# Performance work log

Measured on AMD Instinct MI355X. Metric: run time of the kernel, lower is better.

The kernel has to match this reference:

```python
import jax, jax.numpy as jnp
import numpy as np

EMBED = 1024
NHEAD = 16
HEAD_DIM = EMBED // NHEAD
DFF = 4096
TOP_K = 64
LN_EPS = 1e-5


def _layernorm(x, g, b):
    mu = jnp.mean(x, axis=-1, keepdims=True)
    var = jnp.var(x, axis=-1, keepdims=True)
    return (x - mu) * jax.lax.rsqrt(var + LN_EPS) * g + b


def setup_inputs() -> dict:
    key = jax.random.key(0)
    ks = jax.random.split(key, 12)
    s = 0.02
    return {
        "x": jax.random.normal(ks[0], (2, 2048, EMBED), dtype=jnp.float32),
        "Wq": jax.random.normal(ks[1], (EMBED, EMBED), dtype=jnp.float32) * s,
        "bq": jnp.zeros((EMBED,), jnp.float32),
        "Wk": jax.random.normal(ks[2], (EMBED, EMBED), dtype=jnp.float32) * s,
        "bk": jnp.zeros((EMBED,), jnp.float32),
        "Wv": jax.random.normal(ks[3], (EMBED, EMBED), dtype=jnp.float32) * s,
        "bv": jnp.zeros((EMBED,), jnp.float32),
        "Wo": jax.random.normal(ks[4], (EMBED, EMBED), dtype=jnp.float32) * s,
        "bo": jnp.zeros((EMBED,), jnp.float32),
        "g1": jnp.ones((EMBED,), jnp.float32),
        "be1": jnp.zeros((EMBED,), jnp.float32),
        "g2": jnp.ones((EMBED,), jnp.float32),
        "be2": jnp.zeros((EMBED,), jnp.float32),
        "W1": jax.random.normal(ks[5], (EMBED, DFF), dtype=jnp.float32) * s,
        "b1": jnp.zeros((DFF,), jnp.float32),
        "W2": jax.random.normal(ks[6], (DFF, EMBED), dtype=jnp.float32) * s,
        "b2": jnp.zeros((EMBED,), jnp.float32),
    }


def reference(x, Wq, bq, Wk, bk, Wv, bv, Wo, bo, g1, be1, g2, be2, W1, b1, W2, b2):
    B, N, E = x.shape
    res = x
    h = _layernorm(x, g1, be1)
    # [B, H, N, D]
    q = (h @ Wq + bq).reshape(B, N, NHEAD, HEAD_DIM).transpose(0, 2, 1, 3)
    k = (h @ Wk + bk).reshape(B, N, NHEAD, HEAD_DIM).transpose(0, 2, 1, 3)
    v = (h @ Wv + bv).reshape(B, N, NHEAD, HEAD_DIM).transpose(0, 2, 1, 3)
    scores = jnp.einsum("bhqd,bhkd->bhqk", q, k) / jnp.sqrt(jnp.float32(HEAD_DIM))
    if TOP_K < N:
        topv, _ = jax.lax.top_k(scores, TOP_K)  # [B,H,N,TOP_K]
        thresh = topv[..., -1:, ]
        scores = jnp.where(scores < thresh, -jnp.inf, scores)
    attn = jax.nn.softmax(scores, axis=-1)
    out = jnp.einsum("bhqk,bhkd->bhqd", attn, v)
    out = out.transpose(0, 2, 1, 3).reshape(B, N, E)
    out = out @ Wo + bo
    x1 = res + out  # dropout is identity at eval
    h2 = _layernorm(x1, g2, be2)
    ff = jax.nn.gelu(h2 @ W1 + b1, approximate=False) @ W2 + b2
    return x1 + ff
```

## Files before the change

### kernel.cpp

```cpp
#include <hip/hip_runtime.h>

typedef short short8v __attribute__((ext_vector_type(8)));
typedef float floatx4 __attribute__((ext_vector_type(4)));
typedef unsigned short us4 __attribute__((ext_vector_type(4)));

#define EMB 1024
#define QKVW 3072
#define SEQ 2048
#define NH 16
#define HD 64
#define TOPK 64
#define QBLK 16
#define CAP 128
#define SROW 2056
#define ATTN_SMEM (QBLK * SROW * 2 + QBLK * CAP * 4)

#define GLDS16(gp, lp)                                                        \
  __builtin_amdgcn_global_load_lds(                                           \
      (const __attribute__((address_space(1))) void*)(gp),                    \
      (__attribute__((address_space(3))) void*)(lp), 16, 0, 0)

static __device__ __forceinline__ unsigned short f2b(float f) {
  union { float f; unsigned u; } in; in.f = f;
  unsigned u = in.u;
  return (unsigned short)((u + 0x7FFFu + ((u >> 16) & 1u)) >> 16);
}
static __device__ __forceinline__ float b2f(unsigned short b) {
  union { unsigned u; float f; } o; o.u = ((unsigned)b) << 16;
  return o.f;
}
static __device__ __forceinline__ unsigned mmap(unsigned s) {
  return (s & 0x8000u) ? (~s & 0xFFFFu) : (s | 0x8000u);
}
static __device__ __forceinline__ unsigned short munmap(unsigned u) {
  return (u & 0x8000u) ? (unsigned short)(u ^ 0x8000u) : (unsigned short)(~u & 0xFFFFu);
}

__global__ __launch_bounds__(256) void ln_kernel(const float* __restrict__ X,
    const float* __restrict__ gam, const float* __restrict__ bet,
    unsigned short* __restrict__ H) {
  const int row = blockIdx.x;
  const int tid = threadIdx.x;
  const float4 v = *(const float4*)&X[(size_t)row * EMB + tid * 4];
  float s1 = v.x + v.y + v.z + v.w;
  float s2 = v.x * v.x + v.y * v.y + v.z * v.z + v.w * v.w;
#pragma unroll
  for (int off = 32; off; off >>= 1) { s1 += __shfl_xor(s1, off); s2 += __shfl_xor(s2, off); }
  __shared__ float red[2][4];
  const int w = tid >> 6, l = tid & 63;
  if (l == 0) { red[0][w] = s1; red[1][w] = s2; }
  __syncthreads();
  s1 = red[0][0] + red[0][1] + red[0][2] + red[0][3];
  s2 = red[1][0] + red[1][1] + red[1][2] + red[1][3];
  const float mu = s1 * (1.f / EMB);
  const float var = s2 * (1.f / EMB) - mu * mu;
  const float rs = rsqrtf(var + 1e-5f);
  const float4 gv = *(const float4*)&gam[tid * 4];
  const float4 bv = *(const float4*)&bet[tid * 4];
  us4 o;
  o.x = f2b((v.x - mu) * rs * gv.x + bv.x);
  o.y = f2b((v.y - mu) * rs * gv.y + bv.y);
  o.z = f2b((v.z - mu) * rs * gv.z + bv.z);
  o.w = f2b((v.w - mu) * rs * gv.w + bv.w);
  *(us4*)&H[(size_t)row * EMB + tid * 4] = o;
}

__global__ __launch_bounds__(256) void wcvt_kernel(const float* __restrict__ W,
    unsigned short* __restrict__ WT, int K, int N) {
  __shared__ unsigned short t[64][72];
  const int n0 = blockIdx.x * 64, k0 = blockIdx.y * 64;
  const int tid = threadIdx.x;
#pragma unroll
  for (int i = 0; i < 4; ++i) {
    const int f = i * 256 + tid;
    const int k = f >> 4, n4 = (f & 15) * 4;
    const float4 v = *(const float4*)&W[(size_t)(k0 + k) * N + n0 + n4];
    t[n4 + 0][k] = f2b(v.x);
    t[n4 + 1][k] = f2b(v.y);
    t[n4 + 2][k] = f2b(v.z);
    t[n4 + 3][k] = f2b(v.w);
  }
  __syncthreads();
#pragma unroll
  for (int i = 0; i < 2; ++i) {
    const int f = i * 256 + tid;
    const int n = f >> 3, c8 = (f & 7) * 8;
    short8v o;
#pragma unroll
    for (int j = 0; j < 8; ++j) o[j] = (short)t[n][c8 + j];
    *(short8v*)&WT[(size_t)(n0 + n) * K + k0 + c8] = o;
  }
}

static __device__ __forceinline__ void xcd_tile(int& bm, int& bn) {
  const int gx = gridDim.x;
  const int nwg = gx * gridDim.y;
  const int flat = blockIdx.y * gx + blockIdx.x;
  const int q8 = nwg >> 3;
  const int wg = (flat & 7) * q8 + (flat >> 3);
  bm = (wg / gx) * 128;
  bn = (wg % gx) * 128;
}

template <int EPI>
__global__ __launch_bounds__(256) void gemm_bt4_kernel(
    const unsigned short* __restrict__ A, const unsigned short* __restrict__ BT,
    const float* __restrict__ bias, const float* __restrict__ res,
    void* __restrict__ Cout, int M, int N, int K) {
  __shared__ __align__(16) unsigned short lA[128 * 32];
  __shared__ __align__(16) unsigned short lB[128 * 32];
  const int tid = threadIdx.x;
  const int l = tid & 63, w = tid >> 6;
  const int wm = (w >> 1) * 64, wn = (w & 1) * 64;
  int bm, bn; xcd_tile(bm, bn);
  const int g = l >> 4, r16 = l & 15;
  const int lr = l >> 2, lc = (l & 3) * 8;
  floatx4 acc[4][4] = {};
  for (int kt = 0; kt < K; kt += 32) {
#pragma unroll
    for (int j = 0; j < 2; ++j) {
      GLDS16(&A[(size_t)(bm + w * 32 + j * 16 + lr) * K + kt + lc],
             &lA[(w * 32 + j * 16) * 32]);
      GLDS16(&BT[(size_t)(bn + w * 32 + j * 16 + lr) * K + kt + lc],
             &lB[(w * 32 + j * 16) * 32]);
    }
    __syncthreads();
    short8v a[4], b[4];
#pragma unroll
    for (int m = 0; m < 4; ++m) a[m] = *(const short8v*)&lA[(wm + m * 16 + r16) * 32 + g * 8];
#pragma unroll
    for (int n = 0; n < 4; ++n) b[n] = *(const short8v*)&lB[(wn + n * 16 + r16) * 32 + g * 8];
#pragma unroll
    for (int m = 0; m < 4; ++m)
#pragma unroll
      for (int n = 0; n < 4; ++n)
        acc[m][n] = __builtin_amdgcn_mfma_f32_16x16x32_bf16(a[m], b[n], acc[m][n], 0, 0, 0);
    __syncthreads();
  }
#pragma unroll
  for (int m = 0; m < 4; ++m) {
#pragma unroll
    for (int n = 0; n < 4; ++n) {
#pragma unroll
      for (int r = 0; r < 4; ++r) {
        const int gm = bm + wm + m * 16 + g * 4 + r;
        const int gn = bn + wn + n * 16 + r16;
        float v = acc[m][n][r] + bias[gn];
        if constexpr (EPI == 0) {
          ((unsigned short*)Cout)[(size_t)gm * N + gn] = f2b(v);
        } else if constexpr (EPI == 1) {
          const float ge = 0.5f * v * (1.f + erff(v * 0.70710678118f));
          ((unsigned short*)Cout)[(size_t)gm * N + gn] = f2b(ge);
        } else {
          ((float*)Cout)[(size_t)gm * N + gn] = v + res[(size_t)gm * N + gn];
        }
      }
    }
  }
}

template <int EPI>
__global__ __launch_bounds__(512) void gemm_bt8_kernel(
    const unsigned short* __restrict__ A, const unsigned short* __restrict__ BT,
    const float* __restrict__ bias, const float* __restrict__ res,
    void* __restrict__ Cout, int M, int N, int K) {
  __shared__ __align__(16) unsigned short lA[128 * 32];
  __shared__ __align__(16) unsigned short lB[128 * 32];
  const int tid = threadIdx.x;
  const int l = tid & 63, w = tid >> 6;
  const int wm = (w & 1) * 64, wn = (w >> 1) * 32;
  int bm, bn; xcd_tile(bm, bn);
  const int g = l >> 4, r16 = l & 15;
  const int lr = l >> 2, lc = (l & 3) * 8;
  floatx4 acc[4][2] = {};
  for (int kt = 0; kt < K; kt += 32) {
    GLDS16(&A[(size_t)(bm + w * 16 + lr) * K + kt + lc], &lA[(w * 16) * 32]);
    GLDS16(&BT[(size_t)(bn + w * 16 + lr) * K + kt + lc], &lB[(w * 16) * 32]);
    __syncthreads();
    short8v a[4], b[2];
#pragma unroll
    for (int m = 0; m < 4; ++m) a[m] = *(const short8v*)&lA[(wm + m * 16 + r16) * 32 + g * 8];
#pragma unroll
    for (int n = 0; n < 2; ++n) b[n] = *(const short8v*)&lB[(wn + n * 16 + r16) * 32 + g * 8];
#pragma unroll
    for (int m = 0; m < 4; ++m)
#pragma unroll
      for (int n = 0; n < 2; ++n)
        acc[m][n] = __builtin_amdgcn_mfma_f32_16x16x32_bf16(a[m], b[n], acc[m][n], 0, 0, 0);
    __syncthreads();
  }
#pragma unroll
  for (int m = 0; m < 4; ++m) {
#pragma unroll
    for (int n = 0; n < 2; ++n) {
#pragma unroll
      for (int r = 0; r < 4; ++r) {
        const int gm = bm + wm + m * 16 + g * 4 + r;
        const int gn = bn + wn + n * 16 + r16;
        float v = acc[m][n][r] + bias[gn];
        if constexpr (EPI == 0) {
          ((unsigned short*)Cout)[(size_t)gm * N + gn] = f2b(v);
        } else if constexpr (EPI == 1) {
          const float ge = 0.5f * v * (1.f + erff(v * 0.70710678118f));
          ((unsigned short*)Cout)[(size_t)gm * N + gn] = f2b(ge);
        } else {
          ((float*)Cout)[(size_t)gm * N + gn] = v + res[(size_t)gm * N + gn];
        }
      }
    }
  }
}

__global__ __launch_bounds__(1024, 8) void attn_kernel(
    const unsigned short* __restrict__ qkv, unsigned short* __restrict__ O) {
  extern __shared__ unsigned short smem[];
  unsigned short (*scores)[SROW] = (unsigned short(*)[SROW])smem;
  unsigned* hist = (unsigned*)(smem + QBLK * SROW);

  const int tid = threadIdx.x;
  const int l = tid & 63, w = tid >> 6;
  const int g = l >> 4, r16 = l & 15;
  const int qb = blockIdx.x;
  const int h = blockIdx.y;
  const int bz = blockIdx.z;
  const size_t rowbase = (size_t)bz * SEQ;
  const int hcol = h * HD;

  ((uint2*)hist)[tid] = uint2{0u, 0u};

  {
    const size_t qrow = (rowbase + qb * QBLK + r16) * QKVW + hcol;
    const short8v a0 = *(const short8v*)&qkv[qrow + g * 8];
    const short8v a1 = *(const short8v*)&qkv[qrow + 32 + g * 8];
    const int kbase = w * 128;
#pragma unroll 2
    for (int kti = 0; kti < 8; ++kti) {
      const int key0 = kbase + kti * 16;
      const size_t krow = (rowbase + key0 + r16) * QKVW + 1024 + hcol;
      const short8v b0 = *(const short8v*)&qkv[krow + g * 8];
      const short8v b1 = *(const short8v*)&qkv[krow + 32 + g * 8];
      floatx4 acc = {0.f, 0.f, 0.f, 0.f};
      acc = __builtin_amdgcn_mfma_f32_16x16x32_bf16(a0, b0, acc, 0, 0, 0);
      acc = __builtin_amdgcn_mfma_f32_16x16x32_bf16(a1, b1, acc, 0, 0, 0);
#pragma unroll
      for (int r = 0; r < 4; ++r)
        scores[g * 4 + r][key0 + r16] = (unsigned short)mmap(f2b(acc[r] * 0.125f));
    }
  }
  __syncthreads();

  const unsigned long long ltmask = (1ull << l) - 1ull;
  const int half = l >> 5, dl = l & 31;
  const int q = w;
  unsigned* srow32 = (unsigned*)&scores[q][0];
  unsigned* comp = &hist[q * CAP];

  unsigned ux[16];
  unsigned um = 0;
#pragma unroll
  for (int i = 0; i < 16; ++i) {
    const unsigned x = srow32[l + 64 * i];
    ux[i] = x;
    const unsigned u0 = x & 0xFFFFu, u1 = x >> 16;
    const unsigned mx = (u0 > u1) ? u0 : u1;
    um = (mx > um) ? mx : um;
  }
#pragma unroll
  for (int off = 32; off; off >>= 1) {
    const unsigned o2 = (unsigned)__shfl_xor((int)um, off);
    um = (o2 > um) ? o2 : um;
  }
  const float mf = b2f(munmap(um));

#pragma unroll
  for (int i = 0; i < 16; ++i) {
    const unsigned d0 = um - (ux[i] & 0xFFFFu);
    const unsigned d1 = um - (ux[i] >> 16);
    if (d0 < 256u) atomicAdd(&comp[d0 >> 1], 1u << ((d0 & 1u) * 16));
    if (d1 < 256u) atomicAdd(&comp[d1 >> 1], 1u << ((d1 & 1u) * 16));
  }
  asm volatile("s_waitcnt lgkmcnt(0)" ::: "memory");
  unsigned ut;
  {
    const unsigned w0 = comp[2 * l], w1 = comp[2 * l + 1];
    const unsigned c0 = w0 & 0xFFFFu, c1 = w0 >> 16, c2 = w1 & 0xFFFFu, c3 = w1 >> 16;
    const unsigned s4 = c0 + c1 + c2 + c3;
    unsigned incl = s4;
#pragma unroll
    for (int off = 1; off < 64; off <<= 1) {
      const unsigned t2 = (unsigned)__shfl_up((int)incl, off);
      if (l >= off) incl += t2;
    }
    const unsigned pre = incl - s4;
    unsigned dc = 0xFFFFFFFFu;
    if      (pre + c0 >= TOPK)           dc = 4 * l;
    else if (pre + c0 + c1 >= TOPK)      dc = 4 * l + 1;
    else if (pre + c0 + c1 + c2 >= TOPK) dc = 4 * l + 2;
    else if (incl >= TOPK)               dc = 4 * l + 3;
#pragma unroll
    for (int off = 32; off; off >>= 1) {
      const unsigned o2 = (unsigned)__shfl_xor((int)dc, off);
      dc = (o2 < dc) ? o2 : dc;
    }
    if (dc != 0xFFFFFFFFu) {
      ut = um - dc;
    } else {
      unsigned t = 0;
#pragma unroll 1
      for (int bit = 15; bit >= 0; --bit) {
        const unsigned cand = t | (1u << bit);
        int c = 0;
#pragma unroll
        for (int i = 0; i < 16; ++i) {
          c += __popcll(__ballot((ux[i] & 0xFFFFu) >= cand));
          c += __popcll(__ballot((ux[i] >> 16) >= cand));
        }
        if (c >= TOPK) t = cand;
      }
      ut = t;
    }
  }

  float lsum = 0.f;
  unsigned base = 0;
#pragma unroll
  for (int i = 0; i < 16; ++i) {
    const unsigned u0 = ux[i] & 0xFFFFu, u1 = ux[i] >> 16;
    const bool k0 = (u0 >= ut), k1 = (u1 >= ut);
    const float e0 = k0 ? __expf(b2f(munmap(u0)) - mf) : 0.f;
    const float e1 = k1 ? __expf(b2f(munmap(u1)) - mf) : 0.f;
    lsum += e0 + e1;
    const unsigned key0 = 2 * (l + 64 * i);
    const unsigned long long m0 = __ballot(k0);
    if (k0) {
      const unsigned pos = base + (unsigned)__popcll(m0 & ltmask);
      if (pos < CAP) comp[pos] = (key0 << 16) | (unsigned)f2b(e0);
    }
    base += (unsigned)__popcll(m0);
    const unsigned long long m1 = __ballot(k1);
    if (k1) {
      const unsigned pos = base + (unsigned)__popcll(m1 & ltmask);
      if (pos < CAP) comp[pos] = ((key0 + 1) << 16) | (unsigned)f2b(e1);
    }
    base += (unsigned)__popcll(m1);
  }
#pragma unroll
  for (int off = 32; off; off >>= 1) lsum += __shfl_xor(lsum, off);
  const float rinv = 1.f / lsum;
  const unsigned cntc = (base < CAP) ? base : CAP;

  const unsigned short* vbase = &qkv[rowbase * QKVW + 2048 + hcol + dl * 2];
  float ox = 0.f, oy = 0.f;
#pragma unroll 4
  for (unsigned k = 0; k < 64; k += 2) {
    const unsigned c = comp[k + half];
    const float p = b2f((unsigned short)(c & 0xFFFFu));
    const unsigned idx = c >> 16;
    const unsigned vv = *(const unsigned*)&vbase[(size_t)idx * QKVW];
    ox += p * b2f((unsigned short)(vv & 0xFFFFu));
    oy += p * b2f((unsigned short)(vv >> 16));
  }
#pragma unroll 1
  for (unsigned k = 64; k < cntc; k += 2) {
    const unsigned kk = k + half;
    const unsigned c = (kk < cntc) ? comp[kk] : 0u;
    const float p = b2f((unsigned short)(c & 0xFFFFu));
    const unsigned idx = c >> 16;
    const unsigned vv = *(const unsigned*)&vbase[(size_t)idx * QKVW];
    ox += p * b2f((unsigned short)(vv & 0xFFFFu));
    oy += p * b2f((unsigned short)(vv >> 16));
  }
  ox += __shfl_xor(ox, 32);
  oy += __shfl_xor(oy, 32);
  if (l < 32) {
    const unsigned ow = (unsigned)f2b(ox * rinv) | ((unsigned)f2b(oy * rinv) << 16);
    *(unsigned*)&O[(rowbase + qb * QBLK + q) * EMB + hcol + dl * 2] = ow;
  }
}

extern "C" void kernel_launch(void* const* d_in, const int* in_sizes, int n_in,
                              void* d_out, int out_size, void* d_ws, size_t ws_size,
                              hipStream_t stream) {
  (void)in_sizes; (void)n_in; (void)out_size; (void)ws_size;
  const float* x  = (const float*)d_in[0];
  const float* Wq = (const float*)d_in[1];
  const float* bq = (const float*)d_in[2];
  const float* Wk = (const float*)d_in[3];
  const float* bk = (const float*)d_in[4];
  const float* Wv = (const float*)d_in[5];
  const float* bv = (const float*)d_in[6];
  const float* Wo = (const float*)d_in[7];
  const float* bo = (const float*)d_in[8];
  const float* g1 = (const float*)d_in[9];
  const float* be1 = (const float*)d_in[10];
  const float* g2 = (const float*)d_in[11];
  const float* be2 = (const float*)d_in[12];
  const float* W1 = (const float*)d_in[13];
  const float* b1 = (const float*)d_in[14];
  const float* W2 = (const float*)d_in[15];
  const float* b2 = (const float*)d_in[16];
  float* out = (float*)d_out;

  char* ws = (char*)d_ws;
  float* x1 = (float*)ws;
  unsigned short* hbuf  = (unsigned short*)(ws + ((size_t)16 << 20));
  unsigned short* qkvb  = (unsigned short*)(ws + ((size_t)24 << 20));
  unsigned short* Ob    = (unsigned short*)(ws + ((size_t)48 << 20));
  unsigned short* ff1   = (unsigned short*)(ws + ((size_t)24 << 20));
  float* bqkv           = (float*)(ws + ((size_t)48 << 20));
  unsigned short* WqkvT = (unsigned short*)(ws + ((size_t)56 << 20));
  unsigned short* WoT   = (unsigned short*)(ws + ((size_t)62 << 20));
  unsigned short* W1T   = (unsigned short*)(ws + ((size_t)64 << 20));
  unsigned short* W2T   = (unsigned short*)(ws + ((size_t)72 << 20));

  hipMemcpyAsync(bqkv,        bq, 1024 * 4, hipMemcpyDeviceToDevice, stream);
  hipMemcpyAsync(bqkv + 1024, bk, 1024 * 4, hipMemcpyDeviceToDevice, stream);
  hipMemcpyAsync(bqkv + 2048, bv, 1024 * 4, hipMemcpyDeviceToDevice, stream);

  wcvt_kernel<<<dim3(16, 16), 256, 0, stream>>>(Wq, WqkvT,                1024, 1024);
  wcvt_kernel<<<dim3(16, 16), 256, 0, stream>>>(Wk, WqkvT + 1024 * 1024, 1024, 1024);
  wcvt_kernel<<<dim3(16, 16), 256, 0, stream>>>(Wv, WqkvT + 2048 * 1024, 1024, 1024);
  wcvt_kernel<<<dim3(16, 16), 256, 0, stream>>>(Wo, WoT, 1024, 1024);
  wcvt_kernel<<<dim3(64, 16), 256, 0, stream>>>(W1, W1T, 1024, 4096);
  wcvt_kernel<<<dim3(16, 64), 256, 0, stream>>>(W2, W2T, 4096, 1024);

  ln_kernel<<<dim3(4096), 256, 0, stream>>>(x, g1, be1, hbuf);
  gemm_bt4_kernel<0><<<dim3(24, 32), 256, 0, stream>>>(hbuf, WqkvT, bqkv, nullptr, qkvb,
                                                       4096, QKVW, 1024);
  (void)hipFuncSetAttribute((const void*)attn_kernel,
                            hipFuncAttributeMaxDynamicSharedMemorySize, ATTN_SMEM);
  attn_kernel<<<dim3(128, 16, 2), 1024, ATTN_SMEM, stream>>>(qkvb, Ob);
  gemm_bt8_kernel<2><<<dim3(8, 32), 512, 0, stream>>>(Ob, WoT, bo, x, x1, 4096, 1024, 1024);
  ln_kernel<<<dim3(4096), 256, 0, stream>>>(x1, g2, be2, hbuf);
  gemm_bt4_kernel<1><<<dim3(32, 32), 256, 0, stream>>>(hbuf, W1T, b1, nullptr, ff1,
                                                       4096, 4096, 1024);
  gemm_bt8_kernel<2><<<dim3(8, 32), 512, 0, stream>>>(ff1, W2T, b2, x1, out, 4096, 1024, 4096);
}
```

Measured before the change: 447.6 us.

## Fold softmax scale into Wq and streamline attention top-k softmax and PV gather

The attention scale 1/sqrt(64)*log2(e) is folded into the Wq weights and the bq bias, so the score store can truncate fp32 to bf16 without a multiply and the softmax can use exp2 directly. Three memcpys are replaced with one bias-pack kernel. Inside attention, the row max uses a packed 16-bit max, exponentials are computed without branches and packed with v_cvt_pk_bf16_f32, and the PV gather loads 4 bf16 per lane across 4 key groups instead of 2 per lane across 2. Truncating instead of rounding the scores and scaling the weights before bf16 conversion slightly changes numerics and could shift which keys land at the top-k threshold.

```diff
diff --git a/kernel.cpp b/kernel.cpp
--- a/kernel.cpp
+++ b/kernel.cpp
@@ -3,6 +3,7 @@
 typedef short short8v __attribute__((ext_vector_type(8)));
 typedef float floatx4 __attribute__((ext_vector_type(4)));
 typedef unsigned short us4 __attribute__((ext_vector_type(4)));
+typedef unsigned short us2 __attribute__((ext_vector_type(2)));
 
 #define EMB 1024
 #define QKVW 3072
@@ -13,12 +14,19 @@
 #define QBLK 16
 #define CAP 128
 #define SROW 2056
+#define QSCALE 0.18033688f
 #define ATTN_SMEM (QBLK * SROW * 2 + QBLK * CAP * 4)
 
 #define GLDS16(gp, lp)                                                        \
   __builtin_amdgcn_global_load_lds(                                           \
       (const __attribute__((address_space(1))) void*)(gp),                    \
       (__attribute__((address_space(3))) void*)(lp), 16, 0, 0)
+
+#if __has_builtin(__builtin_amdgcn_exp2f)
+#define EXP2F(x) __builtin_amdgcn_exp2f(x)
+#else
+#define EXP2F(x) exp2f(x)
+#endif
 
 static __device__ __forceinline__ unsigned short f2b(float f) {
   union { float f; unsigned u; } in; in.f = f;
@@ -66,7 +74,7 @@
 }
 
 __global__ __launch_bounds__(256) void wcvt_kernel(const float* __restrict__ W,
-    unsigned short* __restrict__ WT, int K, int N) {
+    unsigned short* __restrict__ WT, int K, int N, float scale) {
   __shared__ unsigned short t[64][72];
   const int n0 = blockIdx.x * 64, k0 = blockIdx.y * 64;
   const int tid = threadIdx.x;
@@ -75,10 +83,10 @@
     const int f = i * 256 + tid;
     const int k = f >> 4, n4 = (f & 15) * 4;
     const float4 v = *(const float4*)&W[(size_t)(k0 + k) * N + n0 + n4];
-    t[n4 + 0][k] = f2b(v.x);
-    t[n4 + 1][k] = f2b(v.y);
-    t[n4 + 2][k] = f2b(v.z);
-    t[n4 + 3][k] = f2b(v.w);
+    t[n4 + 0][k] = f2b(v.x * scale);
+    t[n4 + 1][k] = f2b(v.y * scale);
+    t[n4 + 2][k] = f2b(v.z * scale);
+    t[n4 + 3][k] = f2b(v.w * scale);
   }
   __syncthreads();
 #pragma unroll
@@ -90,6 +98,16 @@
     for (int j = 0; j < 8; ++j) o[j] = (short)t[n][c8 + j];
     *(short8v*)&WT[(size_t)(n0 + n) * K + k0 + c8] = o;
   }
+}
+
+__global__ __launch_bounds__(256) void bias_pack_kernel(const float* __restrict__ bq,
+    const float* __restrict__ bk, const float* __restrict__ bv, float* __restrict__ bqkv) {
+  const int i = blockIdx.x * 256 + threadIdx.x;
+  float v;
+  if (i < 1024) v = bq[i] * QSCALE;
+  else if (i < 2048) v = bk[i - 1024];
+  else v = bv[i - 2048];
+  bqkv[i] = v;
 }
 
 static __device__ __forceinline__ void xcd_tile(int& bm, int& bn) {
@@ -243,28 +261,30 @@
       acc = __builtin_amdgcn_mfma_f32_16x16x32_bf16(a0, b0, acc, 0, 0, 0);
       acc = __builtin_amdgcn_mfma_f32_16x16x32_bf16(a1, b1, acc, 0, 0, 0);
 #pragma unroll
-      for (int r = 0; r < 4; ++r)
-        scores[g * 4 + r][key0 + r16] = (unsigned short)mmap(f2b(acc[r] * 0.125f));
+      for (int r = 0; r < 4; ++r) {
+        union { float f; unsigned u; } cv; cv.f = acc[r];
+        scores[g * 4 + r][key0 + r16] = (unsigned short)mmap(cv.u >> 16);
+      }
     }
   }
   __syncthreads();
 
   const unsigned long long ltmask = (1ull << l) - 1ull;
-  const int half = l >> 5, dl = l & 31;
+  const int quarter = l >> 4, j16 = l & 15;
   const int q = w;
   unsigned* srow32 = (unsigned*)&scores[q][0];
   unsigned* comp = &hist[q * CAP];
 
   unsigned ux[16];
-  unsigned um = 0;
+  us2 mx2 = {0, 0};
 #pragma unroll
   for (int i = 0; i < 16; ++i) {
     const unsigned x = srow32[l + 64 * i];
     ux[i] = x;
-    const unsigned u0 = x & 0xFFFFu, u1 = x >> 16;
-    const unsigned mx = (u0 > u1) ? u0 : u1;
-    um = (mx > um) ? mx : um;
-  }
+    union { unsigned u; us2 v; } c; c.u = x;
+    mx2 = __builtin_elementwise_max(mx2, c.v);
+  }
+  unsigned um = (mx2.x > mx2.y) ? (unsigned)mx2.x : (unsigned)mx2.y;
 #pragma unroll
   for (int off = 32; off; off >>= 1) {
     const unsigned o2 = (unsigned)__shfl_xor((int)um, off);
@@ -327,20 +347,22 @@
   for (int i = 0; i < 16; ++i) {
     const unsigned u0 = ux[i] & 0xFFFFu, u1 = ux[i] >> 16;
     const bool k0 = (u0 >= ut), k1 = (u1 >= ut);
-    const float e0 = k0 ? __expf(b2f(munmap(u0)) - mf) : 0.f;
-    const float e1 = k1 ? __expf(b2f(munmap(u1)) - mf) : 0.f;
-    lsum += e0 + e1;
+    const float e0 = EXP2F(b2f(munmap(u0)) - mf);
+    const float e1 = EXP2F(b2f(munmap(u1)) - mf);
+    lsum += (k0 ? e0 : 0.f) + (k1 ? e1 : 0.f);
+    unsigned pp;
+    asm("v_cvt_pk_bf16_f32 %0, %1, %2" : "=v"(pp) : "v"(e0), "v"(e1));
     const unsigned key0 = 2 * (l + 64 * i);
     const unsigned long long m0 = __ballot(k0);
     if (k0) {
       const unsigned pos = base + (unsigned)__popcll(m0 & ltmask);
-      if (pos < CAP) comp[pos] = (key0 << 16) | (unsigned)f2b(e0);
+      if (pos < CAP) comp[pos] = (key0 << 16) | (pp & 0xFFFFu);
     }
     base += (unsigned)__popcll(m0);
     const unsigned long long m1 = __ballot(k1);
     if (k1) {
       const unsigned pos = base + (unsigned)__popcll(m1 & ltmask);
-      if (pos < CAP) comp[pos] = ((key0 + 1) << 16) | (unsigned)f2b(e1);
+      if (pos < CAP) comp[pos] = ((key0 + 1) << 16) | (pp >> 16);
     }
     base += (unsigned)__popcll(m1);
   }
@@ -349,32 +371,42 @@
   const float rinv = 1.f / lsum;
   const unsigned cntc = (base < CAP) ? base : CAP;
 
-  const unsigned short* vbase = &qkv[rowbase * QKVW + 2048 + hcol + dl * 2];
-  float ox = 0.f, oy = 0.f;
+  const unsigned short* vbase = &qkv[rowbase * QKVW + 2048 + hcol + j16 * 4];
+  float a0 = 0.f, a1 = 0.f, a2 = 0.f, a3 = 0.f;
 #pragma unroll 4
-  for (unsigned k = 0; k < 64; k += 2) {
-    const unsigned c = comp[k + half];
+  for (int k = 0; k < 16; ++k) {
+    const unsigned c = comp[k * 4 + quarter];
     const float p = b2f((unsigned short)(c & 0xFFFFu));
     const unsigned idx = c >> 16;
-    const unsigned vv = *(const unsigned*)&vbase[(size_t)idx * QKVW];
-    ox += p * b2f((unsigned short)(vv & 0xFFFFu));
-    oy += p * b2f((unsigned short)(vv >> 16));
+    const uint2 vv = *(const uint2*)&vbase[(size_t)idx * QKVW];
+    union { unsigned u; float f; } t0, t1, t2, t3;
+    t0.u = vv.x << 16; t1.u = vv.x & 0xFFFF0000u;
+    t2.u = vv.y << 16; t3.u = vv.y & 0xFFFF0000u;
+    a0 += p * t0.f; a1 += p * t1.f; a2 += p * t2.f; a3 += p * t3.f;
   }
 #pragma unroll 1
-  for (unsigned k = 64; k < cntc; k += 2) {
-    const unsigned kk = k + half;
+  for (unsigned k = 64; k < cntc; k += 4) {
+    const unsigned kk = k + quarter;
     const unsigned c = (kk < cntc) ? comp[kk] : 0u;
     const float p = b2f((unsigned short)(c & 0xFFFFu));
     const unsigned idx = c >> 16;
-    const unsigned vv = *(const unsigned*)&vbase[(size_t)idx * QKVW];
-    ox += p * b2f((unsigned short)(vv & 0xFFFFu));
-    oy += p * b2f((unsigned short)(vv >> 16));
-  }
-  ox += __shfl_xor(ox, 32);
-  oy += __shfl_xor(oy, 32);
-  if (l < 32) {
-    const unsigned ow = (unsigned)f2b(ox * rinv) | ((unsigned)f2b(oy * rinv) << 16);
-    *(unsigned*)&O[(rowbase + qb * QBLK + q) * EMB + hcol + dl * 2] = ow;
+    const uint2 vv = *(const uint2*)&vbase[(size_t)idx * QKVW];
+    union { unsigned u; float f; } t0, t1, t2, t3;
+    t0.u = vv.x << 16; t1.u = vv.x & 0xFFFF0000u;
+    t2.u = vv.y << 16; t3.u = vv.y & 0xFFFF0000u;
+    a0 += p * t0.f; a1 += p * t1.f; a2 += p * t2.f; a3 += p * t3.f;
+  }
+  a0 += __shfl_xor(a0, 16); a0 += __shfl_xor(a0, 32);
+  a1 += __shfl_xor(a1, 16); a1 += __shfl_xor(a1, 32);
+  a2 += __shfl_xor(a2, 16); a2 += __shfl_xor(a2, 32);
+  a3 += __shfl_xor(a3, 16); a3 += __shfl_xor(a3, 32);
+  if (l < 16) {
+    unsigned w0, w1;
+    const float r0 = a0 * rinv, r1 = a1 * rinv, r2 = a2 * rinv, r3 = a3 * rinv;
+    asm("v_cvt_pk_bf16_f32 %0, %1, %2" : "=v"(w0) : "v"(r0), "v"(r1));
+    asm("v_cvt_pk_bf16_f32 %0, %1, %2" : "=v"(w1) : "v"(r2), "v"(r3));
+    uint2 ow; ow.x = w0; ow.y = w1;
+    *(uint2*)&O[(rowbase + qb * QBLK + q) * EMB + hcol + j16 * 4] = ow;
   }
 }
 
@@ -413,16 +445,14 @@
   unsigned short* W1T   = (unsigned short*)(ws + ((size_t)64 << 20));
   unsigned short* W2T   = (unsigned short*)(ws + ((size_t)72 << 20));
 
-  hipMemcpyAsync(bqkv,        bq, 1024 * 4, hipMemcpyDeviceToDevice, stream);
-  hipMemcpyAsync(bqkv + 1024, bk, 1024 * 4, hipMemcpyDeviceToDevice, stream);
-  hipMemcpyAsync(bqkv + 2048, bv, 1024 * 4, hipMemcpyDeviceToDevice, stream);
-
-  wcvt_kernel<<<dim3(16, 16), 256, 0, stream>>>(Wq, WqkvT,                1024, 1024);
-  wcvt_kernel<<<dim3(16, 16), 256, 0, stream>>>(Wk, WqkvT + 1024 * 1024, 1024, 1024);
-  wcvt_kernel<<<dim3(16, 16), 256, 0, stream>>>(Wv, WqkvT + 2048 * 1024, 1024, 1024);
-  wcvt_kernel<<<dim3(16, 16), 256, 0, stream>>>(Wo, WoT, 1024, 1024);
-  wcvt_kernel<<<dim3(64, 16), 256, 0, stream>>>(W1, W1T, 1024, 4096);
-  wcvt_kernel<<<dim3(16, 64), 256, 0, stream>>>(W2, W2T, 4096, 1024);
+  bias_pack_kernel<<<dim3(12), 256, 0, stream>>>(bq, bk, bv, bqkv);
+
+  wcvt_kernel<<<dim3(16, 16), 256, 0, stream>>>(Wq, WqkvT,                1024, 1024, QSCALE);
+  wcvt_kernel<<<dim3(16, 16), 256, 0, stream>>>(Wk, WqkvT + 1024 * 1024, 1024, 1024, 1.f);
+  wcvt_kernel<<<dim3(16, 16), 256, 0, stream>>>(Wv, WqkvT + 2048 * 1024, 1024, 1024, 1.f);
+  wcvt_kernel<<<dim3(16, 16), 256, 0, stream>>>(Wo, WoT, 1024, 1024, 1.f);
+  wcvt_kernel<<<dim3(64, 16), 256, 0, stream>>>(W1, W1T, 1024, 4096, 1.f);
+  wcvt_kernel<<<dim3(16, 64), 256, 0, stream>>>(W2, W2T, 4096, 1024, 1.f);
 
   ln_kernel<<<dim3(4096), 256, 0, stream>>>(x, g1, be1, hbuf);
   gemm_bt4_kernel<0><<<dim3(24, 32), 256, 0, stream>>>(hbuf, WqkvT, bqkv, nullptr, qkvb,
```

Measured after the change: 443.2 us. No clear change (-1.0%).
